# Kernel optimization log

Hardware: AMD Instinct MI355X
Metric: run time of the kernel (lower is better)

The kernel has to match this reference:

```python
import jax, jax.numpy as jnp
import numpy as np
import math

B, H, N, K, D = 4, 8, 4096, 32, 8  # batch, heads, points, neighbors, head depth (k_out/H)


def setup_inputs() -> dict:
    key = jax.random.key(0)
    ks = jax.random.split(key, 6)
    return {
        "q": jax.random.normal(ks[0], (B, H, N, 1, D), dtype=jnp.float32),
        "k_mat": jax.random.normal(ks[1], (B, H, N, D, K), dtype=jnp.float32),
        "v": jax.random.normal(ks[2], (B, H, N, K, D), dtype=jnp.float32),
        "re_xyz": jax.random.normal(ks[3], (B, N, K, 3), dtype=jnp.float32),
        "w1": jax.random.normal(ks[4], (3, H), dtype=jnp.float32) * 0.5,  # linear1: 3 -> num_heads
        "b1": jnp.zeros((H,), dtype=jnp.float32),
        "w2": jax.random.normal(ks[5], (3, H * D), dtype=jnp.float32) * 0.5,  # linear2: 3 -> k_out
        "b2": jnp.zeros((H * D,), dtype=jnp.float32),
    }


def reference(q, k_mat, v, re_xyz, w1, b1, w2, b2):
    # pe_ii positional bias on attention scores: [B,N,K,3] -> [B,N,K,H] -> [B,H,N,1,K]
    q_xyz = re_xyz @ w1 + b1
    q_xyz = jnp.transpose(q_xyz, (0, 3, 1, 2))[:, :, :, None, :]
    # energy: [B,H,N,1,D] @ [B,H,N,D,K] -> [B,H,N,1,K]
    energy = jnp.matmul(q, k_mat) + q_xyz
    scale = math.sqrt(q.shape[-1])
    attention = jax.nn.softmax(energy / scale, axis=-1)
    # value positional term: [B,N,K,H*D] raw-reshaped to [B,H,N,K,D] (matches torch .view)
    v_xyz = (re_xyz @ w2 + b2).reshape(v.shape[0], H, v.shape[2], v.shape[3], D)
    v = v + v_xyz
    # [B,H,N,1,K] @ [B,H,N,K,D] -> [B,H,N,1,D] -> [B,N,H,D]
    x = jnp.matmul(attention, v)[:, :, :, 0, :].transpose(0, 2, 1, 3)
    return x
```

## Files before the change

kernel.cpp:

```cpp
#include <hip/hip_runtime.h>
#include <math.h>


#define T_PER_BLOCK 8

__global__ __launch_bounds__(256) void pe_attn_kernel(
    const float* __restrict__ q,
    const float* __restrict__ k_mat,
    const float* __restrict__ v,
    const float* __restrict__ re_xyz,
    const float* __restrict__ w1,
    const float* __restrict__ b1,
    const float* __restrict__ w2,
    const float* __restrict__ b2,
    float* __restrict__ out)
{
    const int tid = threadIdx.x;
    const int t0  = blockIdx.x * T_PER_BLOCK;
    const int it  = tid >> 5;
    const int k   = tid & 31;
    const int t   = t0 + it;
    const int b   = t >> 15;
    const int rem = t & 32767;
    const int h   = rem >> 12;
    const int n   = rem & 4095;

    const float* kbase = k_mat + (size_t)t * 256 + k;
    float kc0 = kbase[0];
    float kc1 = kbase[32];
    float kc2 = kbase[64];
    float kc3 = kbase[96];
    float kc4 = kbase[128];
    float kc5 = kbase[160];
    float kc6 = kbase[192];
    float kc7 = kbase[224];

    const float4 qa = ((const float4*)(q + (size_t)t * 8))[0];
    const float4 qb = ((const float4*)(q + (size_t)t * 8))[1];

    const size_t rxb = ((size_t)((b << 12) + n) * 32 + k) * 3;
    const float rx0 = re_xyz[rxb], rx1 = re_xyz[rxb + 1], rx2 = re_xyz[rxb + 2];

    const int n2 = rem >> 3;
    const int k2 = ((rem & 7) << 2) + (k >> 3);
    const size_t rxb2 = ((size_t)((b << 12) + n2) * 32 + k2) * 3;
    const float s0 = re_xyz[rxb2], s1 = re_xyz[rxb2 + 1], s2 = re_xyz[rxb2 + 2];

    const float* vbase = v + (size_t)t * 256 + k * 8;
    const float4 v0 = ((const float4*)vbase)[0];
    const float4 v1 = ((const float4*)vbase)[1];

    const float wq0 = w1[h], wq1 = w1[8 + h], wq2 = w1[16 + h], bq = b1[h];
    const int c0 = (k & 7) << 3;
    const float4 wr0a = ((const float4*)(w2 + c0))[0];
    const float4 wr0b = ((const float4*)(w2 + c0))[1];
    const float4 wr1a = ((const float4*)(w2 + 64 + c0))[0];
    const float4 wr1b = ((const float4*)(w2 + 64 + c0))[1];
    const float4 wr2a = ((const float4*)(w2 + 128 + c0))[0];
    const float4 wr2b = ((const float4*)(w2 + 128 + c0))[1];
    const float4 bba  = ((const float4*)(b2 + c0))[0];
    const float4 bbb  = ((const float4*)(b2 + c0))[1];

    float e = qa.x * kc0 + qa.y * kc1 + qa.z * kc2 + qa.w * kc3
            + qb.x * kc4 + qb.y * kc5 + qb.z * kc6 + qb.w * kc7;
    e += rx0 * wq0 + rx1 * wq1 + rx2 * wq2 + bq;
    e *= 0.35355339059327373f;
    const float p = __expf(e);

    float s = p;
    #pragma unroll
    for (int off = 16; off; off >>= 1) s += __shfl_xor(s, off);

    float pd[8];
    pd[0] = p * (v0.x + s0 * wr0a.x + s1 * wr1a.x + s2 * wr2a.x + bba.x);
    pd[1] = p * (v0.y + s0 * wr0a.y + s1 * wr1a.y + s2 * wr2a.y + bba.y);
    pd[2] = p * (v0.z + s0 * wr0a.z + s1 * wr1a.z + s2 * wr2a.z + bba.z);
    pd[3] = p * (v0.w + s0 * wr0a.w + s1 * wr1a.w + s2 * wr2a.w + bba.w);
    pd[4] = p * (v1.x + s0 * wr0b.x + s1 * wr1b.x + s2 * wr2b.x + bbb.x);
    pd[5] = p * (v1.y + s0 * wr0b.y + s1 * wr1b.y + s2 * wr2b.y + bbb.y);
    pd[6] = p * (v1.z + s0 * wr0b.z + s1 * wr1b.z + s2 * wr2b.z + bbb.z);
    pd[7] = p * (v1.w + s0 * wr0b.w + s1 * wr1b.w + s2 * wr2b.w + bbb.w);

    {
        const bool hb = (k & 16) != 0;
        #pragma unroll
        for (int j = 0; j < 4; ++j) {
            float send = hb ? pd[j] : pd[j + 4];
            float recv = __shfl_xor(send, 16);
            float keep = hb ? pd[j + 4] : pd[j];
            pd[j] = keep + recv;
        }
    }
    {
        const bool hb = (k & 8) != 0;
        #pragma unroll
        for (int j = 0; j < 2; ++j) {
            float send = hb ? pd[j] : pd[j + 2];
            float recv = __shfl_xor(send, 8);
            float keep = hb ? pd[j + 2] : pd[j];
            pd[j] = keep + recv;
        }
    }
    {
        const bool hb = (k & 4) != 0;
        float send = hb ? pd[0] : pd[1];
        float recv = __shfl_xor(send, 4);
        float keep = hb ? pd[1] : pd[0];
        pd[0] = keep + recv;
    }
    pd[0] += __shfl_xor(pd[0], 2);
    pd[0] += __shfl_xor(pd[0], 1);

    if ((k & 3) == 0) {
        const int d = (k >> 2) & 7;
        out[((size_t)((b << 12) + n) * 8 + h) * 8 + d] =
            pd[0] * __builtin_amdgcn_rcpf(s);
    }
}

extern "C" void kernel_launch(void* const* d_in, const int* in_sizes, int n_in,
                              void* d_out, int out_size, void* d_ws, size_t ws_size,
                              hipStream_t stream) {
    const float* q      = (const float*)d_in[0];
    const float* k_mat  = (const float*)d_in[1];
    const float* v      = (const float*)d_in[2];
    const float* re_xyz = (const float*)d_in[3];
    const float* w1     = (const float*)d_in[4];
    const float* b1     = (const float*)d_in[5];
    const float* w2     = (const float*)d_in[6];
    const float* b2     = (const float*)d_in[7];
    float* out = (float*)d_out;

    dim3 grid(131072 / T_PER_BLOCK), block(256);
    hipLaunchKernelGGL(pe_attn_kernel, grid, block, 0, stream,
                       q, k_mat, v, re_xyz, w1, b1, w2, b2, out);
}
```

Baseline: 286.4 us.

## Stage k_mat tiles into LDS via async global_load_lds, double tokens per block

Loads the key matrix for each block's tokens into shared memory with the direct global-to-LDS load builtin, 16 bytes per lane, instead of eight strided scalar global loads per thread. The block grows to 512 threads covering 16 tokens, and launch bounds become (512,1). Other global loads are reordered so they overlap the async copy before a barrier. The barrier adds synchronisation cost, and the (512,1) launch bound may change register allocation and occupancy.

```diff
diff --git a/kernel.cpp b/kernel.cpp
--- a/kernel.cpp
+++ b/kernel.cpp
@@ -2,9 +2,9 @@
 #include <math.h>
 
 
-#define T_PER_BLOCK 8
+#define T_PER_BLOCK 16
 
-__global__ __launch_bounds__(256) void pe_attn_kernel(
+__global__ __launch_bounds__(512, 1) void pe_attn_kernel(
     const float* __restrict__ q,
     const float* __restrict__ k_mat,
     const float* __restrict__ v,
@@ -15,8 +15,23 @@
     const float* __restrict__ b2,
     float* __restrict__ out)
 {
-    const int tid = threadIdx.x;
-    const int t0  = blockIdx.x * T_PER_BLOCK;
+    __shared__ __align__(16) float lds_k[T_PER_BLOCK * 256];
+
+    const int tid  = threadIdx.x;
+    const int wave = tid >> 6;
+    const int lane = tid & 63;
+    const int t0   = blockIdx.x * T_PER_BLOCK;
+
+    #pragma unroll
+    for (int j = 0; j < 2; ++j) {
+        const int seg = wave * 2 + j;
+        __builtin_amdgcn_global_load_lds(
+            (const __attribute__((address_space(1))) void*)
+                (k_mat + (size_t)t0 * 256 + seg * 256 + lane * 4),
+            (__attribute__((address_space(3))) void*)(lds_k + seg * 256),
+            16, 0, 0);
+    }
+
     const int it  = tid >> 5;
     const int k   = tid & 31;
     const int t   = t0 + it;
@@ -25,18 +40,9 @@
     const int h   = rem >> 12;
     const int n   = rem & 4095;
 
-    const float* kbase = k_mat + (size_t)t * 256 + k;
-    float kc0 = kbase[0];
-    float kc1 = kbase[32];
-    float kc2 = kbase[64];
-    float kc3 = kbase[96];
-    float kc4 = kbase[128];
-    float kc5 = kbase[160];
-    float kc6 = kbase[192];
-    float kc7 = kbase[224];
-
-    const float4 qa = ((const float4*)(q + (size_t)t * 8))[0];
-    const float4 qb = ((const float4*)(q + (size_t)t * 8))[1];
+    const float* vbase = v + (size_t)t * 256 + k * 8;
+    const float4 v0 = ((const float4*)vbase)[0];
+    const float4 v1 = ((const float4*)vbase)[1];
 
     const size_t rxb = ((size_t)((b << 12) + n) * 32 + k) * 3;
     const float rx0 = re_xyz[rxb], rx1 = re_xyz[rxb + 1], rx2 = re_xyz[rxb + 2];
@@ -46,9 +52,8 @@
     const size_t rxb2 = ((size_t)((b << 12) + n2) * 32 + k2) * 3;
     const float s0 = re_xyz[rxb2], s1 = re_xyz[rxb2 + 1], s2 = re_xyz[rxb2 + 2];
 
-    const float* vbase = v + (size_t)t * 256 + k * 8;
-    const float4 v0 = ((const float4*)vbase)[0];
-    const float4 v1 = ((const float4*)vbase)[1];
+    const float4 qa = ((const float4*)(q + (size_t)t * 8))[0];
+    const float4 qb = ((const float4*)(q + (size_t)t * 8))[1];
 
     const float wq0 = w1[h], wq1 = w1[8 + h], wq2 = w1[16 + h], bq = b1[h];
     const int c0 = (k & 7) << 3;
@@ -61,8 +66,17 @@
     const float4 bba  = ((const float4*)(b2 + c0))[0];
     const float4 bbb  = ((const float4*)(b2 + c0))[1];
 
-    float e = qa.x * kc0 + qa.y * kc1 + qa.z * kc2 + qa.w * kc3
-            + qb.x * kc4 + qb.y * kc5 + qb.z * kc6 + qb.w * kc7;
+    __syncthreads();
+
+    const float* kt = lds_k + it * 256;
+    float e = qa.x * kt[k]
+            + qa.y * kt[32  + k]
+            + qa.z * kt[64  + k]
+            + qa.w * kt[96  + k]
+            + qb.x * kt[128 + k]
+            + qb.y * kt[160 + k]
+            + qb.z * kt[192 + k]
+            + qb.w * kt[224 + k];
     e += rx0 * wq0 + rx1 * wq1 + rx2 * wq2 + bq;
     e *= 0.35355339059327373f;
     const float p = __expf(e);
@@ -87,8 +101,7 @@
         for (int j = 0; j < 4; ++j) {
             float send = hb ? pd[j] : pd[j + 4];
             float recv = __shfl_xor(send, 16);
-            float keep = hb ? pd[j + 4] : pd[j];
-            pd[j] = keep + recv;
+            pd[j] = (hb ? pd[j + 4] : pd[j]) + recv;
         }
     }
     {
@@ -97,16 +110,14 @@
         for (int j = 0; j < 2; ++j) {
             float send = hb ? pd[j] : pd[j + 2];
             float recv = __shfl_xor(send, 8);
-            float keep = hb ? pd[j + 2] : pd[j];
-            pd[j] = keep + recv;
+            pd[j] = (hb ? pd[j + 2] : pd[j]) + recv;
         }
     }
     {
         const bool hb = (k & 4) != 0;
         float send = hb ? pd[0] : pd[1];
         float recv = __shfl_xor(send, 4);
-        float keep = hb ? pd[1] : pd[0];
-        pd[0] = keep + recv;
+        pd[0] = (hb ? pd[1] : pd[0]) + recv;
     }
     pd[0] += __shfl_xor(pd[0], 2);
     pd[0] += __shfl_xor(pd[0], 1);
@@ -131,7 +142,7 @@
     const float* b2     = (const float*)d_in[7];
     float* out = (float*)d_out;
 
-    dim3 grid(131072 / T_PER_BLOCK), block(256);
+    dim3 grid(131072 / T_PER_BLOCK), block(512);
     hipLaunchKernelGGL(pe_attn_kernel, grid, block, 0, stream,
                        q, k_mat, v, re_xyz, w1, b1, w2, b2, out);
 }
```

After: 289.3 us. About the same (+1.0%).
